# Performance work log

Hardware: AMD Instinct MI355X
Metric: run time of the kernel (lower is better)

The kernel has to match this reference:

```python
import jax, jax.numpy as jnp
import numpy as np

N = 100000
E = 1600000
CUR = 128
HID = 128
OUT = 128

def setup_inputs() -> dict:
    key = jax.random.key(0)
    ks = jax.random.split(key, 12)
    s = 1.0 / np.sqrt(HID)
    return {
        "x": jax.random.normal(ks[0], (N, CUR), dtype=jnp.float32),
        "edge_index": jax.random.randint(ks[1], (2, E), 0, N, dtype=jnp.int64),
        "edge_weight": jax.random.uniform(ks[2], (E,), dtype=jnp.float32),
        # preprocessor Linear(cur_dim -> hidden_dim), stored as [in, out]
        "W_pre": jax.random.normal(ks[3], (CUR, HID), dtype=jnp.float32) * s,
        "b_pre": jnp.zeros((HID,), dtype=jnp.float32),
        # ARMAConv(hidden -> out), num_stacks=1, num_layers=1 defaults
        "arma_init_w": jax.random.normal(ks[4], (HID, OUT), dtype=jnp.float32) * s,
        "arma_root_w": jax.random.normal(ks[5], (HID, OUT), dtype=jnp.float32) * s,
        "arma_b": jnp.zeros((OUT,), dtype=jnp.float32),
        # SAGEConv(hidden -> out): lin_l on aggregated neighbors (with bias), lin_r on root
        "sage_l_w": jax.random.normal(ks[6], (HID, OUT), dtype=jnp.float32) * s,
        "sage_l_b": jnp.zeros((OUT,), dtype=jnp.float32),
        "sage_r_w": jax.random.normal(ks[7], (HID, OUT), dtype=jnp.float32) * s,
    }

def reference(x, edge_index, edge_weight, W_pre, b_pre, arma_init_w, arma_root_w,
              arma_b, sage_l_w, sage_l_b, sage_r_w):
    row, col = edge_index[0], edge_index[1]  # source -> target

    # preprocessor
    h = x @ W_pre + b_pre  # [N, HID]

    # ---- ARMAConv (num_stacks=1, num_layers=1, act=ReLU) ----
    # gcn_norm without self-loops
    deg = jax.ops.segment_sum(edge_weight, col, num_segments=N)  # in-degree (weighted)
    dis = jnp.where(deg > 0, jax.lax.rsqrt(jnp.maximum(deg, 1e-12)), 0.0)
    norm = dis[row] * edge_weight * dis[col]  # [E]
    t = h @ arma_init_w  # [N, OUT]
    agg = jax.ops.segment_sum(norm[:, None] * t[row], col, num_segments=N)
    arma_out = jax.nn.relu(agg + h @ arma_root_w + arma_b)

    # ---- SAGEConv (mean aggregation, weighted messages, root term) ----
    msg_sum = jax.ops.segment_sum(edge_weight[:, None] * h[row], col, num_segments=N)
    cnt = jax.ops.segment_sum(jnp.ones((E,), dtype=h.dtype), col, num_segments=N)
    mean = msg_sum / jnp.maximum(cnt, 1.0)[:, None]
    sage_out = mean @ sage_l_w + sage_l_b + h @ sage_r_w

    h1 = jax.nn.leaky_relu(arma_out, negative_slope=0.01)
    h2 = jax.nn.leaky_relu(sage_out, negative_slope=0.01)
    return jax.nn.elu(jnp.concatenate([h1, h2], axis=1))
```

## Files before the change

### kernel.cpp

```cpp
#include <hip/hip_runtime.h>
#include <math.h>


typedef __attribute__((ext_vector_type(8))) short short8;
typedef __attribute__((ext_vector_type(4))) float float4v;

#define WQ_SCALE 32767.0f
#define WQ_INV   (1.0f / 32767.0f)
#define NB_BIN   256
#define TSTRIDE  272

__device__ __forceinline__ unsigned f2bf_pack(float a, float b) {
    unsigned ua = __float_as_uint(a);
    unsigned ub = __float_as_uint(b);
    ua += 0x7FFF + ((ua >> 16) & 1);
    ub += 0x7FFF + ((ub >> 16) & 1);
    return (ua >> 16) | (ub & 0xFFFF0000u);
}

__device__ __forceinline__ unsigned short f2bf1(float a) {
    unsigned u = __float_as_uint(a);
    u += 0x7FFF + ((u >> 16) & 1);
    return (unsigned short)(u >> 16);
}

__device__ __forceinline__ float act_leaky_elu(float v) {
    float l = (v >= 0.0f) ? v : 0.01f * v;
    return (l > 0.0f) ? l : (__expf(l) - 1.0f);
}

__device__ __forceinline__ short8 ldfrag(const uint4* __restrict__ pw,
                                         int n, int c, int q) {
    union { uint4 u; short8 s; } r;
    r.u = pw[(size_t)(c * 128 + n) * 4 + q];
    return r.s;
}

__device__ __forceinline__ short8 load_afrag_f32(const float* __restrict__ p) {
    float4 a = ((const float4*)p)[0];
    float4 b = ((const float4*)p)[1];
    union { short8 s8; unsigned u[4]; } r;
    r.u[0] = f2bf_pack(a.x, a.y); r.u[1] = f2bf_pack(a.z, a.w);
    r.u[2] = f2bf_pack(b.x, b.y); r.u[3] = f2bf_pack(b.z, b.w);
    return r.s8;
}

__global__ __launch_bounds__(256)
void k_prep(const float* __restrict__ W0, const float* __restrict__ W1,
            const float* __restrict__ W2, const float* __restrict__ W3,
            const float* __restrict__ W4, uint4* __restrict__ pw) {
    const int mat = blockIdx.x;
    const float* W = (mat == 0) ? W0 : (mat == 1) ? W1 : (mat == 2) ? W2
                   : (mat == 3) ? W3 : W4;
    for (int f = threadIdx.x; f < 2048; f += 256) {
        int q = f & 3, n = (f >> 2) & 127, c = f >> 9;
        int k0 = c * 32 + q * 8;
        unsigned u[4];
        #pragma unroll
        for (int j = 0; j < 4; ++j)
            u[j] = f2bf_pack(W[(k0 + 2 * j) * 128 + n],
                             W[(k0 + 2 * j + 1) * 128 + n]);
        pw[(size_t)mat * 2048 + f] = make_uint4(u[0], u[1], u[2], u[3]);
    }
}

__device__ __forceinline__ void gemm_pre(const float* __restrict__ x,
                                         const uint4* __restrict__ pw,
                                         const float* __restrict__ bpre,
                                         unsigned short* __restrict__ hb,
                                         int N) {
    const int lane = threadIdx.x & 63;
    const int wv = threadIdx.x >> 6;
    const int q = lane >> 4;
    const int m = lane & 15;
    const int cg = wv * 32;
    short8 B[2][4];
    #pragma unroll
    for (int ct = 0; ct < 2; ++ct)
        #pragma unroll
        for (int c = 0; c < 4; ++c)
            B[ct][c] = ldfrag(pw, cg + ct * 16 + m, c, q);
    const float b0 = bpre[cg + m];
    const float b1 = bpre[cg + 16 + m];
    const int rb = blockIdx.x * 128;
    #pragma unroll 2
    for (int rt = 0; rt < 8; ++rt) {
        int row = rb + rt * 16 + m;
        int rc = min(row, N - 1);
        const float* xp = x + (size_t)rc * 128 + q * 8;
        float4v a0 = {0.f, 0.f, 0.f, 0.f}, a1 = {0.f, 0.f, 0.f, 0.f};
        #pragma unroll
        for (int c = 0; c < 4; ++c) {
            short8 a = load_afrag_f32(xp + c * 32);
            a0 = __builtin_amdgcn_mfma_f32_16x16x32_bf16(a, B[0][c], a0, 0, 0, 0);
            a1 = __builtin_amdgcn_mfma_f32_16x16x32_bf16(a, B[1][c], a1, 0, 0, 0);
        }
        #pragma unroll
        for (int r = 0; r < 4; ++r) {
            int ro = rb + rt * 16 + q * 4 + r;
            if (ro < N) {
                hb[(size_t)ro * 128 + cg + m]      = f2bf1(a0[r] + b0);
                hb[(size_t)ro * 128 + cg + 16 + m] = f2bf1(a1[r] + b1);
            }
        }
    }
}

__global__ __launch_bounds__(256)
void k_pre_bin1(const float* __restrict__ x, const uint4* __restrict__ pw,
                const float* __restrict__ bpre, unsigned short* __restrict__ hb,
                int N, int gd,
                const int* __restrict__ ei, int* __restrict__ gcnt,
                unsigned* __restrict__ aux, int* __restrict__ bbase,
                int E, int NBKT) {
    __shared__ int hist[1024];
    if ((int)blockIdx.x >= gd) {
        const int cb = (int)blockIdx.x - gd;
        const int tid = threadIdx.x;
        for (int j = tid; j < NBKT; j += 256) hist[j] = 0;
        __syncthreads();
        const int stride = NB_BIN * 256;
        for (int e = cb * 256 + tid; e < E; e += stride) {
            int col = ei[E + e];
            aux[e] = (unsigned)atomicAdd(&hist[col >> 7], 1);
        }
        __syncthreads();
        for (int j = tid; j < NBKT; j += 256) {
            int h = hist[j];
            int bb = (h > 0) ? atomicAdd(&gcnt[j], h) : 0;
            bbase[cb * 1024 + j] = bb;
        }
        return;
    }
    gemm_pre(x, pw, bpre, hb, N);
}

__global__ __launch_bounds__(256)
void k_pre_cntD(const float* __restrict__ x, const uint4* __restrict__ pw,
                const float* __restrict__ bpre, unsigned short* __restrict__ hb,
                int N, int gd,
                const int* __restrict__ ei, int* __restrict__ cnti,
                int* __restrict__ rank, int E) {
    if ((int)blockIdx.x >= gd) {
        const int stride = ((int)gridDim.x - gd) * 256;
        for (int e = ((int)blockIdx.x - gd) * 256 + (int)threadIdx.x; e < E;
             e += stride) {
            rank[e] = atomicAdd(&cnti[ei[E + e]], 1);
        }
        return;
    }
    gemm_pre(x, pw, bpre, hb, N);
}

__device__ __forceinline__ void scan1024_excl(int* v, int* t) {
    const int tid = threadIdx.x;
    int a0 = v[tid * 4 + 0], a1 = v[tid * 4 + 1];
    int a2 = v[tid * 4 + 2], a3 = v[tid * 4 + 3];
    int ts = a0 + a1 + a2 + a3;
    t[tid] = ts;
    __syncthreads();
    #pragma unroll
    for (int off = 1; off < 256; off <<= 1) {
        int add = (tid >= off) ? t[tid - off] : 0;
        __syncthreads();
        t[tid] += add;
        __syncthreads();
    }
    int ex = t[tid] - ts;
    v[tid * 4 + 0] = ex;
    v[tid * 4 + 1] = ex + a0;
    v[tid * 4 + 2] = ex + a0 + a1;
    v[tid * 4 + 3] = ex + a0 + a1 + a2;
    __syncthreads();
}

__global__ __launch_bounds__(256)
void k_scan1(const int* __restrict__ in, int* __restrict__ out,
             int* __restrict__ blksum, int n) {
    __shared__ int sh[256];
    const int tid = threadIdx.x;
    const int idx = blockIdx.x * 1024 + tid * 4;
    int v0 = (idx + 0 < n) ? in[idx + 0] : 0;
    int v1 = (idx + 1 < n) ? in[idx + 1] : 0;
    int v2 = (idx + 2 < n) ? in[idx + 2] : 0;
    int v3 = (idx + 3 < n) ? in[idx + 3] : 0;
    int tsum = v0 + v1 + v2 + v3;
    sh[tid] = tsum;
    __syncthreads();
    #pragma unroll
    for (int off = 1; off < 256; off <<= 1) {
        int add = (tid >= off) ? sh[tid - off] : 0;
        __syncthreads();
        sh[tid] += add;
        __syncthreads();
    }
    int excl = sh[tid] - tsum;
    if (idx + 0 < n) out[idx + 0] = excl;
    if (idx + 1 < n) out[idx + 1] = excl + v0;
    if (idx + 2 < n) out[idx + 2] = excl + v0 + v1;
    if (idx + 3 < n) out[idx + 3] = excl + v0 + v1 + v2;
    if (tid == 255) blksum[blockIdx.x] = sh[255];
}

__global__ __launch_bounds__(128)
void k_scan2(int* __restrict__ blksum, int nb) {
    __shared__ int sh[128];
    const int tid = threadIdx.x;
    int orig = (tid < nb) ? blksum[tid] : 0;
    sh[tid] = orig;
    __syncthreads();
    #pragma unroll
    for (int off = 1; off < 128; off <<= 1) {
        int add = (tid >= off) ? sh[tid - off] : 0;
        __syncthreads();
        sh[tid] += add;
        __syncthreads();
    }
    if (tid < nb) blksum[tid] = sh[tid] - orig;
}

__global__ __launch_bounds__(256)
void k_bin2(const int* __restrict__ ei, const float* __restrict__ ew,
            const unsigned* __restrict__ aux, const int* __restrict__ gcnt,
            const int* __restrict__ bbase, uint2* __restrict__ binned,
            int E, int NBKT) {
    __shared__ int base[1024];
    __shared__ int tmp[256];
    const int cb = blockIdx.x;
    const int tid = threadIdx.x;
    #pragma unroll
    for (int k = 0; k < 4; ++k) {
        int i = tid * 4 + k;
        base[i] = (i < NBKT) ? gcnt[i] : 0;
    }
    __syncthreads();
    scan1024_excl(base, tmp);
    for (int j = tid; j < NBKT; j += 256) base[j] += bbase[cb * 1024 + j];
    __syncthreads();
    const int stride = NB_BIN * 256;
    for (int e = cb * 256 + tid; e < E; e += stride) {
        int col = ei[E + e];
        int src = ei[e];
        unsigned wq = (unsigned)__builtin_rintf(ew[e] * WQ_SCALE) & 0x7FFFu;
        int pos = base[col >> 7] + (int)aux[e];
        binned[pos] = make_uint2((wq << 17) | (unsigned)src, (unsigned)col);
    }
}

__global__ __launch_bounds__(256)
void k_bktcsr(const uint2* __restrict__ binned, const int* __restrict__ gcnt,
              unsigned* __restrict__ recs, int* __restrict__ rowp,
              float* __restrict__ dis, int N, int E, int NBKT) {
    __shared__ int gb[1024];
    __shared__ int tmp[256];
    __shared__ int cnt[128];
    __shared__ int colbase[128];
    __shared__ unsigned long long wsum[128];
    const int bkt = blockIdx.x;
    const int tid = threadIdx.x;
    #pragma unroll
    for (int k = 0; k < 4; ++k) {
        int i = tid * 4 + k;
        gb[i] = (i < NBKT) ? gcnt[i] : 0;
    }
    if (tid < 128) { cnt[tid] = 0; wsum[tid] = 0ULL; }
    __syncthreads();
    scan1024_excl(gb, tmp);
    const int s = gb[bkt], e = gb[bkt + 1];
    for (int i = s + tid; i < e; i += 256) {
        uint2 r = binned[i];
        int cl = (int)(r.y & 127u);
        atomicAdd(&cnt[cl], 1);
        atomicAdd(&wsum[cl], (unsigned long long)(r.x >> 17));
    }
    __syncthreads();
    if (tid < 128) colbase[tid] = cnt[tid];
    __syncthreads();
    #pragma unroll
    for (int off = 1; off < 128; off <<= 1) {
        int add = 0;
        if (tid < 128 && tid >= off) add = colbase[tid - off];
        __syncthreads();
        if (tid < 128) colbase[tid] += add;
        __syncthreads();
    }
    if (tid < 128) {
        colbase[tid] = s + colbase[tid] - cnt[tid];
        int node = bkt * 128 + tid;
        if (node < N) {
            rowp[node] = colbase[tid];
            float d = (float)wsum[tid] * WQ_INV;
            dis[node] = (wsum[tid] > 0ULL)
                          ? (1.0f / sqrtf(fmaxf(d, 1e-12f))) : 0.0f;
        }
        cnt[tid] = 0;
    }
    if (bkt == 0 && tid == 0) rowp[N] = E;
    __syncthreads();
    for (int i = s + tid; i < e; i += 256) {
        uint2 r = binned[i];
        int cl = (int)(r.y & 127u);
        int rk = atomicAdd(&cnt[cl], 1);
        recs[colbase[cl] + rk] = r.x;
    }
}

__global__ __launch_bounds__(256)
void k_scatterW(const int* __restrict__ ei, const float* __restrict__ ew,
                const int* __restrict__ rowp, const int* __restrict__ blks,
                const int* __restrict__ rank, int2* __restrict__ recs, int E) {
    int e = blockIdx.x * 256 + threadIdx.x;
    if (e < E) {
        int c = ei[E + e];
        int pos = rowp[c] + blks[c >> 10] + rank[e];
        recs[pos] = make_int2(ei[e], __float_as_int(ew[e]));
    }
}

__global__ __launch_bounds__(256)
void k_degsumW(const int* __restrict__ rowp, const int* __restrict__ blks,
               const int2* __restrict__ recs, float* __restrict__ dis, int N) {
    int n = blockIdx.x * 256 + threadIdx.x;
    if (n >= N) return;
    int s  = rowp[n] + blks[n >> 10];
    int eE = rowp[n + 1] + blks[(n + 1) >> 10];
    float d = 0.0f;
    for (int e = s; e < eE; ++e) d += __int_as_float(recs[e].y);
    dis[n] = (d > 0.0f) ? (1.0f / sqrtf(fmaxf(d, 1e-12f))) : 0.0f;
}

template <bool ABS>
__global__ __launch_bounds__(256)
void k_pull(const int* __restrict__ rowp, const int* __restrict__ blks,
            const void* __restrict__ recs_, const float* __restrict__ dis,
            const uint4* __restrict__ hb4, uint4* __restrict__ agb4,
            uint4* __restrict__ mnb4, int N) {
    const int node = blockIdx.x * 4 + (threadIdx.x >> 6);
    if (node >= N) return;
    const int lane = threadIdx.x & 63;
    const int q4 = lane >> 4;
    const int sub = lane & 15;
    int s, eE;
    if (ABS) {
        s  = __builtin_amdgcn_readfirstlane(rowp[node]);
        eE = __builtin_amdgcn_readfirstlane(rowp[node + 1]);
    } else {
        s  = __builtin_amdgcn_readfirstlane(rowp[node] + blks[node >> 10]);
        eE = __builtin_amdgcn_readfirstlane(rowp[node + 1] +
                                            blks[(node + 1) >> 10]);
    }
    const float dcol = dis[node];
    const float im = 1.0f / fmaxf((float)(eE - s), 1.0f);

    float aA[8], aM[8];
    #pragma unroll
    for (int i = 0; i < 8; ++i) { aA[i] = 0.f; aM[i] = 0.f; }

    if (ABS) {
        const unsigned* recs = (const unsigned*)recs_;
        for (int ch = s; ch < eE; ch += 64) {
            unsigned rv64 = (ch + lane < eE) ? recs[ch + lane] : 0u;
            const int kmax = min(16, (eE - ch + 3) >> 2);
            #pragma unroll 2
            for (int k = 0; k < kmax; ++k) {
                unsigned rv = (unsigned)__shfl((int)rv64, k * 4 + q4, 64);
                int src = (int)(rv & 0x1FFFFu);
                float w = (float)(rv >> 17) * WQ_INV;
                float c = dis[src] * w;
                uint4 u = hb4[(size_t)src * 16 + sub];
                float f0 = __uint_as_float(u.x << 16);
                float f1 = __uint_as_float(u.x & 0xFFFF0000u);
                float f2 = __uint_as_float(u.y << 16);
                float f3 = __uint_as_float(u.y & 0xFFFF0000u);
                float f4 = __uint_as_float(u.z << 16);
                float f5 = __uint_as_float(u.z & 0xFFFF0000u);
                float f6 = __uint_as_float(u.w << 16);
                float f7 = __uint_as_float(u.w & 0xFFFF0000u);
                aA[0] = fmaf(c, f0, aA[0]); aM[0] = fmaf(w, f0, aM[0]);
                aA[1] = fmaf(c, f1, aA[1]); aM[1] = fmaf(w, f1, aM[1]);
                aA[2] = fmaf(c, f2, aA[2]); aM[2] = fmaf(w, f2, aM[2]);
                aA[3] = fmaf(c, f3, aA[3]); aM[3] = fmaf(w, f3, aM[3]);
                aA[4] = fmaf(c, f4, aA[4]); aM[4] = fmaf(w, f4, aM[4]);
                aA[5] = fmaf(c, f5, aA[5]); aM[5] = fmaf(w, f5, aM[5]);
                aA[6] = fmaf(c, f6, aA[6]); aM[6] = fmaf(w, f6, aM[6]);
                aA[7] = fmaf(c, f7, aA[7]); aM[7] = fmaf(w, f7, aM[7]);
            }
        }
    } else {
        #pragma unroll 2
        for (int e = s; e < eE; e += 4) {
            int el = e + q4;
            bool ok = el < eE;
            int el2 = ok ? el : (eE - 1);
            int2 rv = ((const int2*)recs_)[el2];
            int src = rv.x;
            float w = __int_as_float(rv.y);
            if (!ok) w = 0.f;
            float c = dis[src] * w;
            uint4 u = hb4[(size_t)src * 16 + sub];
            float f0 = __uint_as_float(u.x << 16);
            float f1 = __uint_as_float(u.x & 0xFFFF0000u);
            float f2 = __uint_as_float(u.y << 16);
            float f3 = __uint_as_float(u.y & 0xFFFF0000u);
            float f4 = __uint_as_float(u.z << 16);
            float f5 = __uint_as_float(u.z & 0xFFFF0000u);
            float f6 = __uint_as_float(u.w << 16);
            float f7 = __uint_as_float(u.w & 0xFFFF0000u);
            aA[0] = fmaf(c, f0, aA[0]); aM[0] = fmaf(w, f0, aM[0]);
            aA[1] = fmaf(c, f1, aA[1]); aM[1] = fmaf(w, f1, aM[1]);
            aA[2] = fmaf(c, f2, aA[2]); aM[2] = fmaf(w, f2, aM[2]);
            aA[3] = fmaf(c, f3, aA[3]); aM[3] = fmaf(w, f3, aM[3]);
            aA[4] = fmaf(c, f4, aA[4]); aM[4] = fmaf(w, f4, aM[4]);
            aA[5] = fmaf(c, f5, aA[5]); aM[5] = fmaf(w, f5, aM[5]);
            aA[6] = fmaf(c, f6, aA[6]); aM[6] = fmaf(w, f6, aM[6]);
            aA[7] = fmaf(c, f7, aA[7]); aM[7] = fmaf(w, f7, aM[7]);
        }
    }

    #pragma unroll
    for (int i = 0; i < 8; ++i) {
        aA[i] += __shfl_xor(aA[i], 32, 64);
        aA[i] += __shfl_xor(aA[i], 16, 64);
        aM[i] += __shfl_xor(aM[i], 32, 64);
        aM[i] += __shfl_xor(aM[i], 16, 64);
    }

    if (q4 == 0) {
        uint4 o;
        o.x = f2bf_pack(aA[0] * dcol, aA[1] * dcol);
        o.y = f2bf_pack(aA[2] * dcol, aA[3] * dcol);
        o.z = f2bf_pack(aA[4] * dcol, aA[5] * dcol);
        o.w = f2bf_pack(aA[6] * dcol, aA[7] * dcol);
        agb4[(size_t)node * 16 + sub] = o;
    } else if (q4 == 1) {
        uint4 o;
        o.x = f2bf_pack(aM[0] * im, aM[1] * im);
        o.y = f2bf_pack(aM[2] * im, aM[3] * im);
        o.z = f2bf_pack(aM[4] * im, aM[5] * im);
        o.w = f2bf_pack(aM[6] * im, aM[7] * im);
        mnb4[(size_t)node * 16 + sub] = o;
    }
}

__global__ __launch_bounds__(512)
void k_final2(const unsigned short* __restrict__ agb,
              const unsigned short* __restrict__ mnb,
              const unsigned short* __restrict__ hb,
              const uint4* __restrict__ pw,
              const float* __restrict__ ab, const float* __restrict__ bsl,
              float* __restrict__ out, int N) {
    __shared__ char lds[3 * 64 * TSTRIDE];
    const int tid = threadIdx.x;
    const int lane = tid & 63;
    const int wv = tid >> 6;
    const bool sg = wv >= 4;
    const int q = lane >> 4;
    const int m = lane & 15;
    const int cg = (wv & 3) * 32;
    const int rb = blockIdx.x * 64;

    uint4 stg[3][2];
    {
        const uint4* s0 = (const uint4*)agb;
        const uint4* s1 = (const uint4*)mnb;
        const uint4* s2 = (const uint4*)hb;
        #pragma unroll
        for (int h = 0; h < 2; ++h) {
            int i = tid + h * 512;
            int row = i >> 4, ch = i & 15;
            size_t g = (size_t)min(rb + row, N - 1) * 16 + ch;
            stg[0][h] = s0[g];
            stg[1][h] = s1[g];
            stg[2][h] = s2[g];
        }
    }

    const uint4* W1 = pw + (size_t)(sg ? 3 : 1) * 2048;
    const uint4* W2 = pw + (size_t)(sg ? 4 : 2) * 2048;
    const float* bias = sg ? bsl : ab;
    short8 B1[2][4], B2[2][4];
    #pragma unroll
    for (int ct = 0; ct < 2; ++ct)
        #pragma unroll
        for (int c = 0; c < 4; ++c) {
            B1[ct][c] = ldfrag(W1, cg + ct * 16 + m, c, q);
            B2[ct][c] = ldfrag(W2, cg + ct * 16 + m, c, q);
        }
    const float b0 = bias[cg + m];
    const float b1 = bias[cg + 16 + m];

    #pragma unroll
    for (int t = 0; t < 3; ++t)
        #pragma unroll
        for (int h = 0; h < 2; ++h) {
            int i = tid + h * 512;
            int row = i >> 4, ch = i & 15;
            *(uint4*)&lds[t * 64 * TSTRIDE + row * TSTRIDE + ch * 16] = stg[t][h];
        }
    __syncthreads();

    const char* A1l = &lds[(sg ? 1 : 0) * 64 * TSTRIDE];
    const char* A2l = &lds[2 * 64 * TSTRIDE];
    float* op = out + (sg ? 128 : 0);
    #pragma unroll 2
    for (int rt = 0; rt < 4; ++rt) {
        const int lrow = rt * 16 + m;
        const char* a1p = A1l + lrow * TSTRIDE + q * 16;
        const char* a2p = A2l + lrow * TSTRIDE + q * 16;
        float4v c0a = {0.f,0.f,0.f,0.f}, c0b = {0.f,0.f,0.f,0.f};
        float4v c1a = {0.f,0.f,0.f,0.f}, c1b = {0.f,0.f,0.f,0.f};
        #pragma unroll
        for (int c = 0; c < 4; ++c) {
            short8 a = *(const short8*)(a1p + c * 64);
            short8 b = *(const short8*)(a2p + c * 64);
            c0a = __builtin_amdgcn_mfma_f32_16x16x32_bf16(a, B1[0][c], c0a, 0, 0, 0);
            c1a = __builtin_amdgcn_mfma_f32_16x16x32_bf16(a, B1[1][c], c1a, 0, 0, 0);
            c0b = __builtin_amdgcn_mfma_f32_16x16x32_bf16(b, B2[0][c], c0b, 0, 0, 0);
            c1b = __builtin_amdgcn_mfma_f32_16x16x32_bf16(b, B2[1][c], c1b, 0, 0, 0);
        }
        #pragma unroll
        for (int r = 0; r < 4; ++r) {
            int ro = rb + rt * 16 + q * 4 + r;
            if (ro < N) {
                float v0 = c0a[r] + c0b[r] + b0;
                float v1 = c1a[r] + c1b[r] + b1;
                if (!sg) { v0 = fmaxf(v0, 0.f); v1 = fmaxf(v1, 0.f); }
                else     { v0 = act_leaky_elu(v0); v1 = act_leaky_elu(v1); }
                op[(size_t)ro * 256 + cg + m]      = v0;
                op[(size_t)ro * 256 + cg + 16 + m] = v1;
            }
        }
    }
}

extern "C" void kernel_launch(void* const* d_in, const int* in_sizes, int n_in,
                              void* d_out, int out_size, void* d_ws, size_t ws_size,
                              hipStream_t stream) {
    const float* x    = (const float*)d_in[0];
    const int*   ei   = (const int*)d_in[1];
    const float* ew   = (const float*)d_in[2];
    const float* Wpre = (const float*)d_in[3];
    const float* bpre = (const float*)d_in[4];
    const float* Wai  = (const float*)d_in[5];
    const float* War  = (const float*)d_in[6];
    const float* ab   = (const float*)d_in[7];
    const float* Wsl  = (const float*)d_in[8];
    const float* bsl  = (const float*)d_in[9];
    const float* Wsr  = (const float*)d_in[10];

    const int N = in_sizes[0] / 128;
    const int E = in_sizes[2];
    const size_t NF = (size_t)N * 128;
    const int NBKT = (N + 127) >> 7;
    const bool packed = (N <= 130944);

    char* p = (char*)d_ws;
    auto take = [&p](size_t bytes) {
        char* r = p;
        p += (bytes + 255) & ~(size_t)255;
        return r;
    };
    unsigned short* hb  = (unsigned short*)take(NF * 2);
    unsigned short* agb = (unsigned short*)take(NF * 2);
    unsigned short* mnb = (unsigned short*)take(NF * 2);
    unsigned* recs = (unsigned*)take(packed ? (size_t)E * 4 : (size_t)E * 8);
    int*   rowp = (int*)take((size_t)(N + 1) * 4);
    float* dis  = (float*)take((size_t)N * 4);
    int*   cti  = (int*)take((size_t)(N + 1) * 4);
    int*   blks = (int*)take(128 * 4);
    int*   gcnt = (int*)take(1025 * 4);
    uint4* pw   = (uint4*)take((size_t)5 * 2048 * 16);

    size_t binB = (size_t)E * 8;
    uint2* binned = (NF * 2 >= binB) ? (uint2*)agb : (uint2*)take(binB);
    size_t auxB = ((size_t)E * 4 + 255) & ~(size_t)255;
    size_t bbB  = (size_t)NB_BIN * 1024 * 4;
    unsigned* aux; int* bbase;
    if (NF * 2 >= auxB + bbB) {
        aux = (unsigned*)mnb;
        bbase = (int*)((char*)mnb + auxB);
    } else {
        aux = (unsigned*)take((size_t)E * 4);
        bbase = (int*)take(bbB);
    }

    const int gd = (N + 127) / 128;
    const int gf = (N + 63) / 64;
    const int ge = (E + 255) / 256;
    const int gv = (N + 255) / 256;
    const int ns = N + 1;
    const int nb = (ns + 1023) / 1024;

    k_prep<<<5, 256, 0, stream>>>(Wpre, Wai, War, Wsl, Wsr, pw);

    if (packed) {
        hipMemsetAsync(gcnt, 0, (size_t)(NBKT + 1) * 4, stream);
        k_pre_bin1<<<gd + NB_BIN, 256, 0, stream>>>(x, pw, bpre, hb, N, gd,
                                                    ei, gcnt, aux, bbase,
                                                    E, NBKT);
        k_bin2<<<NB_BIN, 256, 0, stream>>>(ei, ew, aux, gcnt, bbase,
                                           binned, E, NBKT);
        k_bktcsr<<<NBKT, 256, 0, stream>>>(binned, gcnt, recs, rowp, dis,
                                           N, E, NBKT);
        k_pull<true><<<(N + 3) / 4, 256, 0, stream>>>(rowp, blks, recs, dis,
            (const uint4*)hb, (uint4*)agb, (uint4*)mnb, N);
    } else {
        hipMemsetAsync(cti, 0, (size_t)(N + 1) * 4, stream);
        k_pre_cntD<<<gd + 2048, 256, 0, stream>>>(x, pw, bpre, hb, N, gd,
                                                  ei, cti, (int*)aux, E);
        k_scan1<<<nb, 256, 0, stream>>>(cti, rowp, blks, ns);
        k_scan2<<<1, 128, 0, stream>>>(blks, nb);
        k_scatterW<<<ge, 256, 0, stream>>>(ei, ew, rowp, blks, (int*)aux,
                                           (int2*)recs, E);
        k_degsumW<<<gv, 256, 0, stream>>>(rowp, blks, (const int2*)recs,
                                          dis, N);
        k_pull<false><<<(N + 3) / 4, 256, 0, stream>>>(rowp, blks, recs, dis,
            (const uint4*)hb, (uint4*)agb, (uint4*)mnb, N);
    }

    k_final2<<<gf, 512, 0, stream>>>(agb, mnb, hb, pw, ab, bsl,
                                     (float*)d_out, N);
}
```

Baseline: 343.2 us.

## Fuse neighbor pull aggregation with final MFMA projection in packed path

In the packed-record path, the separate pull kernel and final GEMM kernel are merged into one kernel. Each 512-thread block aggregates its 64 nodes into LDS as bf16 and then runs the MFMA projections directly from LDS. This removes the global write and re-read of the aggregated and mean buffers plus one launch. The cost is less parallelism in the gather phase: 64 nodes per block with 8 nodes per wave handled serially, and LDS-limited occupancy during the latency-bound gather.

```diff
diff --git a/kernel.cpp b/kernel.cpp
--- a/kernel.cpp
+++ b/kernel.cpp
@@ -329,10 +329,9 @@
     dis[n] = (d > 0.0f) ? (1.0f / sqrtf(fmaxf(d, 1e-12f))) : 0.0f;
 }
 
-template <bool ABS>
 __global__ __launch_bounds__(256)
 void k_pull(const int* __restrict__ rowp, const int* __restrict__ blks,
-            const void* __restrict__ recs_, const float* __restrict__ dis,
+            const int2* __restrict__ recs, const float* __restrict__ dis,
             const uint4* __restrict__ hb4, uint4* __restrict__ agb4,
             uint4* __restrict__ mnb4, int N) {
     const int node = blockIdx.x * 4 + (threadIdx.x >> 6);
@@ -340,15 +339,9 @@
     const int lane = threadIdx.x & 63;
     const int q4 = lane >> 4;
     const int sub = lane & 15;
-    int s, eE;
-    if (ABS) {
-        s  = __builtin_amdgcn_readfirstlane(rowp[node]);
-        eE = __builtin_amdgcn_readfirstlane(rowp[node + 1]);
-    } else {
-        s  = __builtin_amdgcn_readfirstlane(rowp[node] + blks[node >> 10]);
-        eE = __builtin_amdgcn_readfirstlane(rowp[node + 1] +
+    int s  = __builtin_amdgcn_readfirstlane(rowp[node] + blks[node >> 10]);
+    int eE = __builtin_amdgcn_readfirstlane(rowp[node + 1] +
                                             blks[(node + 1) >> 10]);
-    }
     const float dcol = dis[node];
     const float im = 1.0f / fmaxf((float)(eE - s), 1.0f);
 
@@ -356,45 +349,107 @@
     #pragma unroll
     for (int i = 0; i < 8; ++i) { aA[i] = 0.f; aM[i] = 0.f; }
 
-    if (ABS) {
-        const unsigned* recs = (const unsigned*)recs_;
-        for (int ch = s; ch < eE; ch += 64) {
-            unsigned rv64 = (ch + lane < eE) ? recs[ch + lane] : 0u;
-            const int kmax = min(16, (eE - ch + 3) >> 2);
-            #pragma unroll 2
-            for (int k = 0; k < kmax; ++k) {
-                unsigned rv = (unsigned)__shfl((int)rv64, k * 4 + q4, 64);
-                int src = (int)(rv & 0x1FFFFu);
-                float w = (float)(rv >> 17) * WQ_INV;
-                float c = dis[src] * w;
-                uint4 u = hb4[(size_t)src * 16 + sub];
-                float f0 = __uint_as_float(u.x << 16);
-                float f1 = __uint_as_float(u.x & 0xFFFF0000u);
-                float f2 = __uint_as_float(u.y << 16);
-                float f3 = __uint_as_float(u.y & 0xFFFF0000u);
-                float f4 = __uint_as_float(u.z << 16);
-                float f5 = __uint_as_float(u.z & 0xFFFF0000u);
-                float f6 = __uint_as_float(u.w << 16);
-                float f7 = __uint_as_float(u.w & 0xFFFF0000u);
-                aA[0] = fmaf(c, f0, aA[0]); aM[0] = fmaf(w, f0, aM[0]);
-                aA[1] = fmaf(c, f1, aA[1]); aM[1] = fmaf(w, f1, aM[1]);
-                aA[2] = fmaf(c, f2, aA[2]); aM[2] = fmaf(w, f2, aM[2]);
-                aA[3] = fmaf(c, f3, aA[3]); aM[3] = fmaf(w, f3, aM[3]);
-                aA[4] = fmaf(c, f4, aA[4]); aM[4] = fmaf(w, f4, aM[4]);
-                aA[5] = fmaf(c, f5, aA[5]); aM[5] = fmaf(w, f5, aM[5]);
-                aA[6] = fmaf(c, f6, aA[6]); aM[6] = fmaf(w, f6, aM[6]);
-                aA[7] = fmaf(c, f7, aA[7]); aM[7] = fmaf(w, f7, aM[7]);
-            }
-        }
-    } else {
+    #pragma unroll 2
+    for (int e = s; e < eE; e += 4) {
+        int el = e + q4;
+        bool ok = el < eE;
+        int el2 = ok ? el : (eE - 1);
+        int2 rv = recs[el2];
+        int src = rv.x;
+        float w = __int_as_float(rv.y);
+        if (!ok) w = 0.f;
+        float c = dis[src] * w;
+        uint4 u = hb4[(size_t)src * 16 + sub];
+        float f0 = __uint_as_float(u.x << 16);
+        float f1 = __uint_as_float(u.x & 0xFFFF0000u);
+        float f2 = __uint_as_float(u.y << 16);
+        float f3 = __uint_as_float(u.y & 0xFFFF0000u);
+        float f4 = __uint_as_float(u.z << 16);
+        float f5 = __uint_as_float(u.z & 0xFFFF0000u);
+        float f6 = __uint_as_float(u.w << 16);
+        float f7 = __uint_as_float(u.w & 0xFFFF0000u);
+        aA[0] = fmaf(c, f0, aA[0]); aM[0] = fmaf(w, f0, aM[0]);
+        aA[1] = fmaf(c, f1, aA[1]); aM[1] = fmaf(w, f1, aM[1]);
+        aA[2] = fmaf(c, f2, aA[2]); aM[2] = fmaf(w, f2, aM[2]);
+        aA[3] = fmaf(c, f3, aA[3]); aM[3] = fmaf(w, f3, aM[3]);
+        aA[4] = fmaf(c, f4, aA[4]); aM[4] = fmaf(w, f4, aM[4]);
+        aA[5] = fmaf(c, f5, aA[5]); aM[5] = fmaf(w, f5, aM[5]);
+        aA[6] = fmaf(c, f6, aA[6]); aM[6] = fmaf(w, f6, aM[6]);
+        aA[7] = fmaf(c, f7, aA[7]); aM[7] = fmaf(w, f7, aM[7]);
+    }
+
+    #pragma unroll
+    for (int i = 0; i < 8; ++i) {
+        aA[i] += __shfl_xor(aA[i], 32, 64);
+        aA[i] += __shfl_xor(aA[i], 16, 64);
+        aM[i] += __shfl_xor(aM[i], 32, 64);
+        aM[i] += __shfl_xor(aM[i], 16, 64);
+    }
+
+    if (q4 == 0) {
+        uint4 o;
+        o.x = f2bf_pack(aA[0] * dcol, aA[1] * dcol);
+        o.y = f2bf_pack(aA[2] * dcol, aA[3] * dcol);
+        o.z = f2bf_pack(aA[4] * dcol, aA[5] * dcol);
+        o.w = f2bf_pack(aA[6] * dcol, aA[7] * dcol);
+        agb4[(size_t)node * 16 + sub] = o;
+    } else if (q4 == 1) {
+        uint4 o;
+        o.x = f2bf_pack(aM[0] * im, aM[1] * im);
+        o.y = f2bf_pack(aM[2] * im, aM[3] * im);
+        o.z = f2bf_pack(aM[4] * im, aM[5] * im);
+        o.w = f2bf_pack(aM[6] * im, aM[7] * im);
+        mnb4[(size_t)node * 16 + sub] = o;
+    }
+}
+
+__global__ __launch_bounds__(512)
+void k_pullfin(const int* __restrict__ rowp, const unsigned* __restrict__ recs,
+               const float* __restrict__ dis,
+               const unsigned short* __restrict__ hb,
+               const uint4* __restrict__ pw,
+               const float* __restrict__ ab, const float* __restrict__ bsl,
+               float* __restrict__ out, int N) {
+    __shared__ char lds[3 * 64 * TSTRIDE];
+    const int tid = threadIdx.x;
+    const int lane = tid & 63;
+    const int wv = tid >> 6;
+    const bool sg = wv >= 4;
+    const int q4 = lane >> 4;
+    const int sub = lane & 15;
+    const int cg = (wv & 3) * 32;
+    const int rb = blockIdx.x * 64;
+    const uint4* hb4 = (const uint4*)hb;
+
+    #pragma unroll
+    for (int h = 0; h < 2; ++h) {
+        int i = tid + h * 512;
+        int row = i >> 4, ch = i & 15;
+        uint4 v = hb4[(size_t)min(rb + row, N - 1) * 16 + ch];
+        *(uint4*)&lds[2 * 64 * TSTRIDE + row * TSTRIDE + ch * 16] = v;
+    }
+
+    for (int j = 0; j < 8; ++j) {
+        const int lrow = wv * 8 + j;
+        const int node = rb + lrow;
+        if (node >= N) break;
+        int s  = __builtin_amdgcn_readfirstlane(rowp[node]);
+        int eE = __builtin_amdgcn_readfirstlane(rowp[node + 1]);
+        const float dcol = dis[node];
+        const float im = 1.0f / fmaxf((float)(eE - s), 1.0f);
+
+        float aA[8], aM[8];
+        #pragma unroll
+        for (int i = 0; i < 8; ++i) { aA[i] = 0.f; aM[i] = 0.f; }
+
         #pragma unroll 2
         for (int e = s; e < eE; e += 4) {
             int el = e + q4;
             bool ok = el < eE;
             int el2 = ok ? el : (eE - 1);
-            int2 rv = ((const int2*)recs_)[el2];
-            int src = rv.x;
-            float w = __int_as_float(rv.y);
+            unsigned rv = recs[el2];
+            int src = (int)(rv & 0x1FFFFu);
+            float w = (float)(rv >> 17) * WQ_INV;
             if (!ok) w = 0.f;
             float c = dis[src] * w;
             uint4 u = hb4[(size_t)src * 16 + sub];
@@ -415,30 +470,79 @@
             aA[6] = fmaf(c, f6, aA[6]); aM[6] = fmaf(w, f6, aM[6]);
             aA[7] = fmaf(c, f7, aA[7]); aM[7] = fmaf(w, f7, aM[7]);
         }
-    }
-
-    #pragma unroll
-    for (int i = 0; i < 8; ++i) {
-        aA[i] += __shfl_xor(aA[i], 32, 64);
-        aA[i] += __shfl_xor(aA[i], 16, 64);
-        aM[i] += __shfl_xor(aM[i], 32, 64);
-        aM[i] += __shfl_xor(aM[i], 16, 64);
-    }
-
-    if (q4 == 0) {
-        uint4 o;
-        o.x = f2bf_pack(aA[0] * dcol, aA[1] * dcol);
-        o.y = f2bf_pack(aA[2] * dcol, aA[3] * dcol);
-        o.z = f2bf_pack(aA[4] * dcol, aA[5] * dcol);
-        o.w = f2bf_pack(aA[6] * dcol, aA[7] * dcol);
-        agb4[(size_t)node * 16 + sub] = o;
-    } else if (q4 == 1) {
-        uint4 o;
-        o.x = f2bf_pack(aM[0] * im, aM[1] * im);
-        o.y = f2bf_pack(aM[2] * im, aM[3] * im);
-        o.z = f2bf_pack(aM[4] * im, aM[5] * im);
-        o.w = f2bf_pack(aM[6] * im, aM[7] * im);
-        mnb4[(size_t)node * 16 + sub] = o;
+
+        #pragma unroll
+        for (int i = 0; i < 8; ++i) {
+            aA[i] += __shfl_xor(aA[i], 32, 64);
+            aA[i] += __shfl_xor(aA[i], 16, 64);
+            aM[i] += __shfl_xor(aM[i], 32, 64);
+            aM[i] += __shfl_xor(aM[i], 16, 64);
+        }
+
+        if (q4 == 0) {
+            uint4 o;
+            o.x = f2bf_pack(aA[0] * dcol, aA[1] * dcol);
+            o.y = f2bf_pack(aA[2] * dcol, aA[3] * dcol);
+            o.z = f2bf_pack(aA[4] * dcol, aA[5] * dcol);
+            o.w = f2bf_pack(aA[6] * dcol, aA[7] * dcol);
+            *(uint4*)&lds[lrow * TSTRIDE + sub * 16] = o;
+        } else if (q4 == 1) {
+            uint4 o;
+            o.x = f2bf_pack(aM[0] * im, aM[1] * im);
+            o.y = f2bf_pack(aM[2] * im, aM[3] * im);
+            o.z = f2bf_pack(aM[4] * im, aM[5] * im);
+            o.w = f2bf_pack(aM[6] * im, aM[7] * im);
+            *(uint4*)&lds[64 * TSTRIDE + lrow * TSTRIDE + sub * 16] = o;
+        }
+    }
+
+    const uint4* W1 = pw + (size_t)(sg ? 3 : 1) * 2048;
+    const uint4* W2 = pw + (size_t)(sg ? 4 : 2) * 2048;
+    const float* bias = sg ? bsl : ab;
+    short8 B1[2][4], B2[2][4];
+    #pragma unroll
+    for (int ct = 0; ct < 2; ++ct)
+        #pragma unroll
+        for (int c = 0; c < 4; ++c) {
+            B1[ct][c] = ldfrag(W1, cg + ct * 16 + sub, c, q4);
+            B2[ct][c] = ldfrag(W2, cg + ct * 16 + sub, c, q4);
+        }
+    const float b0 = bias[cg + sub];
+    const float b1 = bias[cg + 16 + sub];
+
+    __syncthreads();
+
+    const char* A1l = &lds[(sg ? 1 : 0) * 64 * TSTRIDE];
+    const char* A2l = &lds[2 * 64 * TSTRIDE];
+    float* op = out + (sg ? 128 : 0);
+    #pragma unroll 2
+    for (int rt = 0; rt < 4; ++rt) {
+        const int lrow = rt * 16 + sub;
+        const char* a1p = A1l + lrow * TSTRIDE + q4 * 16;
+        const char* a2p = A2l + lrow * TSTRIDE + q4 * 16;
+        float4v c0a = {0.f,0.f,0.f,0.f}, c0b = {0.f,0.f,0.f,0.f};
+        float4v c1a = {0.f,0.f,0.f,0.f}, c1b = {0.f,0.f,0.f,0.f};
+        #pragma unroll
+        for (int c = 0; c < 4; ++c) {
+            short8 a = *(const short8*)(a1p + c * 64);
+            short8 b = *(const short8*)(a2p + c * 64);
+            c0a = __builtin_amdgcn_mfma_f32_16x16x32_bf16(a, B1[0][c], c0a, 0, 0, 0);
+            c1a = __builtin_amdgcn_mfma_f32_16x16x32_bf16(a, B1[1][c], c1a, 0, 0, 0);
+            c0b = __builtin_amdgcn_mfma_f32_16x16x32_bf16(b, B2[0][c], c0b, 0, 0, 0);
+            c1b = __builtin_amdgcn_mfma_f32_16x16x32_bf16(b, B2[1][c], c1b, 0, 0, 0);
+        }
+        #pragma unroll
+        for (int r = 0; r < 4; ++r) {
+            int ro = rb + rt * 16 + q4 * 4 + r;
+            if (ro < N) {
+                float v0 = c0a[r] + c0b[r] + b0;
+                float v1 = c1a[r] + c1b[r] + b1;
+                if (!sg) { v0 = fmaxf(v0, 0.f); v1 = fmaxf(v1, 0.f); }
+                else     { v0 = act_leaky_elu(v0); v1 = act_leaky_elu(v1); }
+                op[(size_t)ro * 256 + cg + sub]      = v0;
+                op[(size_t)ro * 256 + cg + 16 + sub] = v1;
+            }
+        }
     }
 }
 
@@ -602,8 +706,8 @@
                                            binned, E, NBKT);
         k_bktcsr<<<NBKT, 256, 0, stream>>>(binned, gcnt, recs, rowp, dis,
                                            N, E, NBKT);
-        k_pull<true><<<(N + 3) / 4, 256, 0, stream>>>(rowp, blks, recs, dis,
-            (const uint4*)hb, (uint4*)agb, (uint4*)mnb, N);
+        k_pullfin<<<gf, 512, 0, stream>>>(rowp, recs, dis, hb, pw, ab, bsl,
+                                          (float*)d_out, N);
     } else {
         hipMemsetAsync(cti, 0, (size_t)(N + 1) * 4, stream);
         k_pre_cntD<<<gd + 2048, 256, 0, stream>>>(x, pw, bpre, hb, N, gd,
@@ -614,10 +718,10 @@
                                            (int2*)recs, E);
         k_degsumW<<<gv, 256, 0, stream>>>(rowp, blks, (const int2*)recs,
                                           dis, N);
-        k_pull<false><<<(N + 3) / 4, 256, 0, stream>>>(rowp, blks, recs, dis,
-            (const uint4*)hb, (uint4*)agb, (uint4*)mnb, N);
-    }
-
-    k_final2<<<gf, 512, 0, stream>>>(agb, mnb, hb, pw, ab, bsl,
-                                     (float*)d_out, N);
-}
+        k_pull<<<(N + 3) / 4, 256, 0, stream>>>(rowp, blks, (const int2*)recs,
+                                                dis, (const uint4*)hb,
+                                                (uint4*)agb, (uint4*)mnb, N);
+        k_final2<<<gf, 512, 0, stream>>>(agb, mnb, hb, pw, ab, bsl,
+                                         (float*)d_out, N);
+    }
+}
```

Measured after the change: 364.6 us. 1.06x slower.
